# Optimization experiments

Measured on AMD Instinct MI355X. Metric: run time of the kernel, lower is better.

The kernel has to match this reference:

```python
import jax, jax.numpy as jnp
import numpy as np

DIM = 128
NUM_LAYERS = 5
EPS = 1e-5


def setup_inputs() -> dict:
    key = jax.random.key(0)
    ks = jax.random.split(key, 16)
    N, E, D = 50000, 640000, DIM
    x = jax.random.uniform(ks[0], (N, 3), dtype=jnp.float32)
    edge_index = jax.random.randint(ks[1], (2, E), 0, N, dtype=jnp.int64)
    norm = jax.random.uniform(ks[2], (E,), dtype=jnp.float32)
    s3 = 1.0 / np.sqrt(3.0)
    sd = 1.0 / np.sqrt(D)
    return {
        "x": x,
        "edge_index": edge_index,
        "norm": norm,
        "W_enc": jax.random.uniform(ks[3], (D, 3), jnp.float32, -s3, s3),
        "bn_e_gamma": jnp.ones((D,), jnp.float32),
        "bn_e_beta": jnp.zeros((D,), jnp.float32),
        "W_ih": jax.random.uniform(ks[4], (3 * D, D), jnp.float32, -sd, sd),
        "W_hh": jax.random.uniform(ks[5], (3 * D, D), jnp.float32, -sd, sd),
        "b_ih": jax.random.uniform(ks[6], (3 * D,), jnp.float32, -sd, sd),
        "b_hh": jax.random.uniform(ks[7], (3 * D,), jnp.float32, -sd, sd),
        "W_dec": jax.random.uniform(ks[8], (D // 2, D), jnp.float32, -sd, sd),
        "bn_d_gamma": jnp.ones((D // 2,), jnp.float32),
        "bn_d_beta": jnp.zeros((D // 2,), jnp.float32),
        "W_dec2": jax.random.uniform(ks[9], (1, D // 2), jnp.float32, -sd * np.sqrt(2.0), sd * np.sqrt(2.0)),
    }


def batchnorm(h, gamma, beta):
    # training-mode BatchNorm1d: biased batch stats over the node dimension
    mu = jnp.mean(h, axis=0)
    var = jnp.var(h, axis=0)
    return (h - mu) * jax.lax.rsqrt(var + EPS) * gamma + beta


def gru_cell(inp, hid, W_ih, W_hh, b_ih, b_hh):
    gi = inp @ W_ih.T + b_ih  # [N, 3D]
    gh = hid @ W_hh.T + b_hh
    D = hid.shape[1]
    i_r, i_z, i_n = gi[:, :D], gi[:, D:2 * D], gi[:, 2 * D:]
    h_r, h_z, h_n = gh[:, :D], gh[:, D:2 * D], gh[:, 2 * D:]
    r = jax.nn.sigmoid(i_r + h_r)
    z = jax.nn.sigmoid(i_z + h_z)
    n = jnp.tanh(i_n + r * h_n)
    return (1.0 - z) * n + z * hid


def reference(x, edge_index, norm, W_enc, bn_e_gamma, bn_e_beta, W_ih, W_hh, b_ih, b_hh, W_dec, bn_d_gamma, bn_d_beta, W_dec2):
    N = x.shape[0]
    src, dst = edge_index[0], edge_index[1]
    # encode
    h = jax.nn.relu(batchnorm(x @ W_enc.T, bn_e_gamma, bn_e_beta))  # [N, D]
    h_sum = h
    prev_h = h
    for _ in range(NUM_LAYERS):
        # neighborhood aggregation: scatter-add of norm-weighted source features
        msg = norm[:, None] * prev_h[src]  # [E, D]
        h_agg = jax.ops.segment_sum(msg, dst, num_segments=N)  # [N, D]
        h_sum = h_sum + h_agg
        prev_h = gru_cell(h_agg, prev_h, W_ih, W_hh, b_ih, b_hh)
    z = h_sum / (NUM_LAYERS + 1)  # mean over stacked h_list
    # decode
    y = jax.nn.relu(batchnorm(z @ W_dec.T, bn_d_gamma, bn_d_beta))
    y = y @ W_dec2.T  # [N, 1]
    return y.reshape(-1)
```

## Files before the change

kernel.cpp:

```cpp
#include <hip/hip_runtime.h>

#define DD 128

typedef _Float16 f16x8 __attribute__((ext_vector_type(8)));
typedef unsigned short u16x8 __attribute__((ext_vector_type(8)));
typedef float f32x4 __attribute__((ext_vector_type(4)));

__device__ __forceinline__ float sigmoidf_(float v){ return 1.f/(1.f+__expf(-v)); }
__device__ __forceinline__ float tanhf_(float v){
  float e2 = __expf(2.f*v);
  return 1.f - 2.f/(e2 + 1.f);
}
__device__ __forceinline__ float h2f(unsigned short u){
  _Float16 h; __builtin_memcpy(&h, &u, 2); return (float)h;
}
__device__ __forceinline__ unsigned short f2h(float v){
  _Float16 h = (_Float16)v; unsigned short u; __builtin_memcpy(&u, &h, 2); return u;
}

#define PREP_B 416
__global__ void __launch_bounds__(256) k_pre1(
        const float* __restrict__ W_ih, const float* __restrict__ W_hh,
        const float* __restrict__ W_dec, const float* __restrict__ x,
        const float* __restrict__ W_enc, const int* __restrict__ dst,
        unsigned short* __restrict__ Wih_h, unsigned short* __restrict__ Whh_h,
        float* __restrict__ Wt_dec, float* __restrict__ h0, float* __restrict__ stats,
        int* __restrict__ counts, int N, int E){
  const int tid = threadIdx.x;
  const int gb = blockIdx.x;
  const int TOT = 384*128;
  if (gb < PREP_B){
    int idx = gb*256 + tid;
    if (idx < 2*TOT){
      const float* W = (idx < TOT) ? W_ih : W_hh;
      unsigned short* D = (idx < TOT) ? Wih_h : Whh_h;
      int fi = (idx < TOT) ? idx : idx - TOT;
      int t = fi & 7;
      int l = (fi >> 3) & 63;
      int ks = (fi >> 9) & 3;
      int nt = fi >> 11;
      int fg = nt / 3, gate = nt % 3;
      int j = gate*128 + fg*16 + (l & 15);
      int k = ks*32 + ((l >> 4) & 3)*8 + t;
      D[fi] = f2h(W[j*128 + k]);
    } else if (idx < 2*TOT + 64*128){
      int t2 = idx - 2*TOT;
      int j = t2 / 128, k = t2 % 128;
      int o = ((k>>2)*64 + j)*4 + (k&3);
      Wt_dec[o] = W_dec[t2];
    }
  } else if (gb < PREP_B + 256){
    const int b = gb - PREP_B;
    const int f = tid & 127;
    const int sub = tid >> 7;
    const float w0 = W_enc[f*3], w1 = W_enc[f*3+1], w2 = W_enc[f*3+2];
    const int chunk = (N + 255) / 256;
    const int n0 = b * chunk;
    const int n1 = (n0 + chunk < N) ? (n0 + chunk) : N;
    float s = 0.f, q = 0.f;
    for (int n = n0 + sub; n < n1; n += 2){
      float x0 = x[n*3], x1 = x[n*3+1], x2 = x[n*3+2];
      float h = x0*w0 + x1*w1 + x2*w2;
      h0[(size_t)n*DD + f] = h;
      s += h; q += h*h;
    }
    atomicAdd(&stats[f], s);
    atomicAdd(&stats[DD+f], q);
  } else {
    int e = (gb - PREP_B - 256)*256 + tid;
    if (e < E) atomicAdd(&counts[dst[e]], 1);
  }
}

__global__ void __launch_bounds__(256) k_scan_part(const int* __restrict__ counts,
                                                   int* __restrict__ partials, int N){
  int i = blockIdx.x*256 + threadIdx.x;
  int v = (i < N) ? counts[i] : 0;
  #pragma unroll
  for (int off = 32; off > 0; off >>= 1) v += __shfl_down(v, off, 64);
  __shared__ int red[4];
  if ((threadIdx.x & 63) == 0) red[threadIdx.x >> 6] = v;
  __syncthreads();
  if (threadIdx.x == 0) partials[blockIdx.x] = red[0]+red[1]+red[2]+red[3];
}

__global__ void __launch_bounds__(256) k_scan_mid(int* __restrict__ partials, int P,
                                                  int* __restrict__ offsets, int N){
  __shared__ int lds[4];
  __shared__ int carry_s;
  const int lane = threadIdx.x & 63, wid = threadIdx.x >> 6;
  if (threadIdx.x == 0) carry_s = 0;
  __syncthreads();
  for (int base = 0; base < P; base += 256){
    int i = base + threadIdx.x;
    int v = (i < P) ? partials[i] : 0;
    int orig = v;
    #pragma unroll
    for (int off = 1; off < 64; off <<= 1){
      int u = __shfl_up(v, off, 64);
      if (lane >= off) v += u;
    }
    if (lane == 63) lds[wid] = v;
    __syncthreads();
    if (threadIdx.x == 0){
      int s = carry_s;
      for (int k = 0; k < 4; k++){ int t = lds[k]; lds[k] = s; s += t; }
      carry_s = s;
    }
    __syncthreads();
    int excl = v - orig + lds[wid];
    if (i < P) partials[i] = excl;
    __syncthreads();
  }
  if (threadIdx.x == 0) offsets[N] = carry_s;
}

__global__ void __launch_bounds__(256) k_scan_expand(const int* __restrict__ counts,
        const int* __restrict__ partials, int* __restrict__ offsets,
        int* __restrict__ cursors, int N){
  int i = blockIdx.x*256 + threadIdx.x;
  int v = (i < N) ? counts[i] : 0;
  int orig = v;
  const int lane = threadIdx.x & 63, wid = threadIdx.x >> 6;
  #pragma unroll
  for (int off = 1; off < 64; off <<= 1){
    int u = __shfl_up(v, off, 64);
    if (lane >= off) v += u;
  }
  __shared__ int lds[4];
  if (lane == 63) lds[wid] = v;
  __syncthreads();
  int wbase = 0;
  for (int k = 0; k < wid; k++) wbase += lds[k];
  int excl = partials[blockIdx.x] + wbase + v - orig;
  if (i < N){ offsets[i] = excl; cursors[i] = excl; }
}

__global__ void __launch_bounds__(256) k_pre2(
        const float* __restrict__ h0, const float* __restrict__ gamma,
        const float* __restrict__ beta, const float* __restrict__ stats,
        unsigned short* __restrict__ ph, unsigned short* __restrict__ hbn,
        const int* __restrict__ src, const int* __restrict__ dst,
        const float* __restrict__ norm, int* __restrict__ cursors,
        int2* __restrict__ csr, int N, int E, int AB){
  const int tid = threadIdx.x;
  if ((int)blockIdx.x < AB){
    int idx = blockIdx.x*256 + tid;
    if (idx >= N*DD) return;
    int f = idx & (DD-1);
    float invN = 1.f / (float)N;
    float mu = stats[f] * invN;
    float var = stats[DD+f] * invN - mu*mu;
    float v = (h0[idx] - mu) * rsqrtf(var + 1e-5f) * gamma[f] + beta[f];
    v = fmaxf(v, 0.f);
    unsigned short hv = f2h(v);
    ph[idx] = hv;
    hbn[idx] = hv;
  } else {
    int e = ((int)blockIdx.x - AB)*256 + tid;
    if (e >= E) return;
    int p = atomicAdd(&cursors[dst[e]], 1);
    union { float f; int i; } c; c.f = norm[e];
    csr[p] = make_int2(src[e], c.i);
  }
}

__global__ void __launch_bounds__(256, 4) k_layer(
        const unsigned short* __restrict__ phc,
        unsigned short* __restrict__ phn,
        unsigned short* __restrict__ agg_out,
        const int* __restrict__ offsets, const int2* __restrict__ csr,
        const unsigned short* __restrict__ Wih_h, const unsigned short* __restrict__ Whh_h,
        const float* __restrict__ b_ih, const float* __restrict__ b_hh, int N){
  __shared__ unsigned short s_a[32*DD];
  const int tid = threadIdx.x;
  const int n0 = blockIdx.x * 32;

  {
    const int slot = tid >> 4;
    const int q    = tid & 15;
    #pragma unroll
    for (int pass = 0; pass < 2; pass++){
      const int m = slot + pass*16;
      const int n = n0 + m;
      float acc[8];
      #pragma unroll
      for (int t = 0; t < 8; t++) acc[t] = 0.f;
      if (n < N){
        const int s0 = offsets[n], s1 = offsets[n+1];
        int i = s0;
        for (; i + 8 <= s1; i += 8){
          int2 ed[8]; u16x8 R[8];
          #pragma unroll
          for (int u = 0; u < 8; u++) ed[u] = csr[i+u];
          #pragma unroll
          for (int u = 0; u < 8; u++) R[u] = *(const u16x8*)(phc + (size_t)ed[u].x*DD + q*8);
          #pragma unroll
          for (int u = 0; u < 8; u++){
            union { int i; float f; } c; c.i = ed[u].y;
            #pragma unroll
            for (int t = 0; t < 8; t++)
              acc[t] = fmaf(c.f, h2f((unsigned short)R[u][t]), acc[t]);
          }
        }
        if (i + 4 <= s1){
          int2 ed[4]; u16x8 R[4];
          #pragma unroll
          for (int u = 0; u < 4; u++) ed[u] = csr[i+u];
          #pragma unroll
          for (int u = 0; u < 4; u++) R[u] = *(const u16x8*)(phc + (size_t)ed[u].x*DD + q*8);
          #pragma unroll
          for (int u = 0; u < 4; u++){
            union { int i; float f; } c; c.i = ed[u].y;
            #pragma unroll
            for (int t = 0; t < 8; t++)
              acc[t] = fmaf(c.f, h2f((unsigned short)R[u][t]), acc[t]);
          }
          i += 4;
        }
        for (; i < s1; i++){
          int2 ed = csr[i];
          union { int i; float f; } c; c.i = ed.y;
          u16x8 R = *(const u16x8*)(phc + (size_t)ed.x*DD + q*8);
          #pragma unroll
          for (int t = 0; t < 8; t++)
            acc[t] = fmaf(c.f, h2f((unsigned short)R[t]), acc[t]);
        }
      }
      u16x8 vh;
      #pragma unroll
      for (int t = 0; t < 8; t++) vh[t] = f2h(acc[t]);
      if (n < N)
        *(u16x8*)(agg_out + (size_t)n*DD + q*8) = vh;
      const int cc = q ^ (m & 7);
      *(u16x8*)(s_a + m*DD + cc*8) = vh;
    }
  }
  __syncthreads();

  const int w = tid >> 6, l = tid & 63, ar = l & 15, aq = l >> 4;
  int r0 = n0 + ar;      if (r0 >= N) r0 = N-1;
  int r1 = n0 + 16 + ar; if (r1 >= N) r1 = N-1;
  const size_t p0 = (size_t)r0*DD + aq*8;
  const size_t p1 = (size_t)r1*DD + aq*8;
  const int sw = ar & 7;

  for (int g = 0; g < 2; g++){
    const int fg = w*2 + g;
    f32x4 acc_i[2][3], acc_h[2][3];
    #pragma unroll
    for (int ta = 0; ta < 2; ta++)
      #pragma unroll
      for (int t = 0; t < 3; t++){
        acc_i[ta][t] = (f32x4){0.f,0.f,0.f,0.f};
        acc_h[ta][t] = (f32x4){0.f,0.f,0.f,0.f};
      }

    #pragma unroll
    for (int ks = 0; ks < 4; ks++){
      const int c = (ks*4 + aq) ^ sw;
      f16x8 ih0 = *(const f16x8*)(s_a + ar*DD       + c*8);
      f16x8 ih1 = *(const f16x8*)(s_a + (16+ar)*DD  + c*8);
      f16x8 hh0 = *(const f16x8*)(phc + p0 + ks*32);
      f16x8 hh1 = *(const f16x8*)(phc + p1 + ks*32);
      #pragma unroll
      for (int t = 0; t < 3; t++){
        size_t bo = ((size_t)((fg*3 + t)*4 + ks)*64 + l)*8;
        f16x8 bih = *(const f16x8*)(Wih_h + bo);
        f16x8 bhh = *(const f16x8*)(Whh_h + bo);
        acc_i[0][t] = __builtin_amdgcn_mfma_f32_16x16x32_f16(ih0, bih, acc_i[0][t], 0, 0, 0);
        acc_i[1][t] = __builtin_amdgcn_mfma_f32_16x16x32_f16(ih1, bih, acc_i[1][t], 0, 0, 0);
        acc_h[0][t] = __builtin_amdgcn_mfma_f32_16x16x32_f16(hh0, bhh, acc_h[0][t], 0, 0, 0);
        acc_h[1][t] = __builtin_amdgcn_mfma_f32_16x16x32_f16(hh1, bhh, acc_h[1][t], 0, 0, 0);
      }
    }

    const int f = fg*16 + ar;
    const float bir = b_ih[f], biz = b_ih[128+f], bin_ = b_ih[256+f];
    const float bhr = b_hh[f], bhz = b_hh[128+f], bhn = b_hh[256+f];
    #pragma unroll
    for (int ta = 0; ta < 2; ta++){
      #pragma unroll
      for (int r = 0; r < 4; r++){
        int n = n0 + ta*16 + aq*4 + r;
        if (n < N){
          float sir = acc_i[ta][0][r] + bir, shr = acc_h[ta][0][r] + bhr;
          float siz = acc_i[ta][1][r] + biz, shz = acc_h[ta][1][r] + bhz;
          float sin_ = acc_i[ta][2][r] + bin_, shn = acc_h[ta][2][r] + bhn;
          float rr = sigmoidf_(sir + shr);
          float zz = sigmoidf_(siz + shz);
          float nn = tanhf_(sin_ + rr*shn);
          size_t o = (size_t)n*DD + f;
          float hp = h2f(phc[o]);
          float h = (1.f - zz)*nn + zz*hp;
          phn[o] = f2h(h);
        }
      }
    }
  }
}

__global__ void __launch_bounds__(256) k_dec1(const unsigned short* __restrict__ hbn,
        const unsigned short* __restrict__ aggs, size_t NF,
        const unsigned short* __restrict__ ph5,
        const int* __restrict__ offsets, const int2* __restrict__ csr,
        const float* __restrict__ Wt_dec, float* __restrict__ y1,
        float* __restrict__ stats_d, int N){
  __shared__ float zs[32][DD];
  const int tid = threadIdx.x;
  const int n0 = blockIdx.x * 32;

  {
    const int slot = tid >> 4;
    const int q    = tid & 15;
    #pragma unroll
    for (int pass = 0; pass < 2; pass++){
      const int m = slot + pass*16;
      const int n = n0 + m;
      float acc[8];
      #pragma unroll
      for (int t = 0; t < 8; t++) acc[t] = 0.f;
      if (n < N){
        size_t o = (size_t)n*DD + q*8;
        u16x8 hb = *(const u16x8*)(hbn + o);
        #pragma unroll
        for (int t = 0; t < 8; t++) acc[t] = h2f(hb[t]);
        #pragma unroll
        for (int l = 0; l < 4; l++){
          u16x8 ag = *(const u16x8*)(aggs + l*NF + o);
          #pragma unroll
          for (int t = 0; t < 8; t++) acc[t] += h2f(ag[t]);
        }
        const int s0 = offsets[n], s1 = offsets[n+1];
        int i = s0;
        for (; i + 8 <= s1; i += 8){
          int2 ed[8]; u16x8 R[8];
          #pragma unroll
          for (int u = 0; u < 8; u++) ed[u] = csr[i+u];
          #pragma unroll
          for (int u = 0; u < 8; u++) R[u] = *(const u16x8*)(ph5 + (size_t)ed[u].x*DD + q*8);
          #pragma unroll
          for (int u = 0; u < 8; u++){
            union { int i; float f; } c; c.i = ed[u].y;
            #pragma unroll
            for (int t = 0; t < 8; t++)
              acc[t] = fmaf(c.f, h2f((unsigned short)R[u][t]), acc[t]);
          }
        }
        if (i + 4 <= s1){
          int2 ed[4]; u16x8 R[4];
          #pragma unroll
          for (int u = 0; u < 4; u++) ed[u] = csr[i+u];
          #pragma unroll
          for (int u = 0; u < 4; u++) R[u] = *(const u16x8*)(ph5 + (size_t)ed[u].x*DD + q*8);
          #pragma unroll
          for (int u = 0; u < 4; u++){
            union { int i; float f; } c; c.i = ed[u].y;
            #pragma unroll
            for (int t = 0; t < 8; t++)
              acc[t] = fmaf(c.f, h2f((unsigned short)R[u][t]), acc[t]);
          }
          i += 4;
        }
        for (; i < s1; i++){
          int2 ed = csr[i];
          union { int i; float f; } c; c.i = ed.y;
          u16x8 R = *(const u16x8*)(ph5 + (size_t)ed.x*DD + q*8);
          #pragma unroll
          for (int t = 0; t < 8; t++)
            acc[t] = fmaf(c.f, h2f((unsigned short)R[t]), acc[t]);
        }
      }
      #pragma unroll
      for (int t = 0; t < 8; t++) zs[m][q*8 + t] = acc[t] * (1.f/6.f);
    }
  }
  __syncthreads();

  const int w = tid >> 6, j = tid & 63;
  float s = 0.f, q = 0.f;
  #pragma unroll
  for (int it = 0; it < 8; it++){
    const int m = w*8 + it;
    const int n = n0 + m;
    if (n < N){
      float acc = 0.f;
      for (int k = 0; k < DD; k += 4){
        float4 wv = *(const float4*)(Wt_dec + ((size_t)(k>>2)*64 + j)*4);
        acc += zs[m][k]*wv.x + zs[m][k+1]*wv.y + zs[m][k+2]*wv.z + zs[m][k+3]*wv.w;
      }
      y1[(size_t)n*64 + j] = acc;
      s += acc; q += acc*acc;
    }
  }
  __shared__ float red[2][4][64];
  red[0][w][j] = s; red[1][w][j] = q;
  __syncthreads();
  if (w == 0){
    s = red[0][0][j] + red[0][1][j] + red[0][2][j] + red[0][3][j];
    q = red[1][0][j] + red[1][1][j] + red[1][2][j] + red[1][3][j];
    float* st = stats_d + (size_t)(blockIdx.x & 7)*128;
    atomicAdd(&st[j], s);
    atomicAdd(&st[64+j], q);
  }
}

__global__ void __launch_bounds__(256) k_dec2(const float* __restrict__ y1,
        const float* __restrict__ gamma, const float* __restrict__ beta,
        const float* __restrict__ W_dec2, const float* __restrict__ stats_d,
        float* __restrict__ out, int N){
  const int j = threadIdx.x & 63;
  const int g = threadIdx.x >> 6;
  const int n = blockIdx.x*4 + g;
  if (n >= N) return;
  float ssum = 0.f, qsum = 0.f;
  #pragma unroll
  for (int c = 0; c < 8; c++){
    ssum += stats_d[c*128 + j];
    qsum += stats_d[c*128 + 64 + j];
  }
  float invN = 1.f / (float)N;
  float mu = ssum * invN;
  float var = qsum * invN - mu*mu;
  float v = (y1[(size_t)n*64 + j] - mu) * rsqrtf(var + 1e-5f) * gamma[j] + beta[j];
  v = fmaxf(v, 0.f) * W_dec2[j];
  for (int off = 32; off > 0; off >>= 1) v += __shfl_down(v, off, 64);
  if (j == 0) out[n] = v;
}

extern "C" void kernel_launch(void* const* d_in, const int* in_sizes, int n_in,
                              void* d_out, int out_size, void* d_ws, size_t ws_size,
                              hipStream_t stream) {
  const int N = in_sizes[0] / 3;
  const int E = in_sizes[1] / 2;
  const int P = (N + 255) / 256;
  const int HIST_B = (E + 255) / 256;
  const int AB = (N*DD + 255) / 256;

  const float* x     = (const float*)d_in[0];
  const int*   ei    = (const int*)d_in[1];
  const int*   src   = ei;
  const int*   dst   = ei + E;
  const float* norm  = (const float*)d_in[2];
  const float* W_enc = (const float*)d_in[3];
  const float* g_e   = (const float*)d_in[4];
  const float* b_e   = (const float*)d_in[5];
  const float* W_ih  = (const float*)d_in[6];
  const float* W_hh  = (const float*)d_in[7];
  const float* b_ih  = (const float*)d_in[8];
  const float* b_hh  = (const float*)d_in[9];
  const float* W_dec = (const float*)d_in[10];
  const float* g_d   = (const float*)d_in[11];
  const float* b_d   = (const float*)d_in[12];
  const float* W_dec2= (const float*)d_in[13];
  float* out = (float*)d_out;

  float* ws = (float*)d_ws;
  const size_t NF = (size_t)N * DD;
  float* scr    = ws;
  float* stats  = scr + NF;
  float* Wt_dec = stats + 1280;
  unsigned short* Wih_h = (unsigned short*)(Wt_dec + 64*128);
  unsigned short* Whh_h = Wih_h + 384*128;
  unsigned short* ph_A  = Whh_h + 384*128;
  unsigned short* ph_B  = ph_A + NF;
  unsigned short* hbn   = ph_B + NF;
  unsigned short* aggs  = hbn + NF;
  int*   counts  = (int*)(aggs + 4*NF);
  int*   offsets = counts + N;
  int*   cursors = offsets + N + 1;
  int*   partials= cursors + N;
  int2*  csr     = (int2*)(partials + P);
  float* y1 = scr;

  hipMemsetAsync(stats, 0, 1280*sizeof(float), stream);
  hipMemsetAsync(counts, 0, (size_t)N*sizeof(int), stream);

  k_pre1<<<PREP_B + 256 + HIST_B, 256, 0, stream>>>(
      W_ih, W_hh, W_dec, x, W_enc, dst,
      Wih_h, Whh_h, Wt_dec, scr, stats, counts, N, E);
  k_scan_part<<<P, 256, 0, stream>>>(counts, partials, N);
  k_scan_mid<<<1, 256, 0, stream>>>(partials, P, offsets, N);
  k_scan_expand<<<P, 256, 0, stream>>>(counts, partials, offsets, cursors, N);
  k_pre2<<<AB + HIST_B, 256, 0, stream>>>(
      scr, g_e, b_e, stats, ph_A, hbn,
      src, dst, norm, cursors, csr, N, E, AB);

  unsigned short* phh_c = ph_A;
  unsigned short* phh_n = ph_B;
  for (int l = 0; l < 4; l++){
    k_layer<<<(N + 31)/32, 256, 0, stream>>>(phh_c, phh_n, aggs + (size_t)l*NF,
                                             offsets, csr,
                                             Wih_h, Whh_h, b_ih, b_hh, N);
    unsigned short* t = phh_c; phh_c = phh_n; phh_n = t;
  }

  k_dec1<<<(N + 31)/32, 256, 0, stream>>>(hbn, aggs, NF, phh_c, offsets, csr,
                                          Wt_dec, y1, stats + 256, N);
  k_dec2<<<(N + 3)/4, 256, 0, stream>>>(y1, g_d, b_d, W_dec2, stats + 256, out, N);
}
```

Measured before the change: 514.9 us.

## Halve node tile to 16 rows and use MFMA for decoder projection

The per-layer kernel now handles 16 nodes per block instead of 32, with one gather pass per thread and half the MFMA accumulators, and the launch bound allows 5 blocks per CU. This is meant to raise occupancy and parallelism for the latency-bound gather. The decoder first stage is rewritten to store z as fp16 in swizzled shared memory and compute the 128→64 projection with fp16 MFMA against a pre-packed W_dec, replacing the scalar fp32 dot-product loop and shared-memory reduction. Each weight fragment is now reused across only 16 rows, so weight loads per node double, and z is rounded to fp16 before the projection.

```diff
diff --git a/kernel.cpp b/kernel.cpp
--- a/kernel.cpp
+++ b/kernel.cpp
@@ -24,7 +24,7 @@
         const float* __restrict__ W_dec, const float* __restrict__ x,
         const float* __restrict__ W_enc, const int* __restrict__ dst,
         unsigned short* __restrict__ Wih_h, unsigned short* __restrict__ Whh_h,
-        float* __restrict__ Wt_dec, float* __restrict__ h0, float* __restrict__ stats,
+        unsigned short* __restrict__ Wd_h, float* __restrict__ h0, float* __restrict__ stats,
         int* __restrict__ counts, int N, int E){
   const int tid = threadIdx.x;
   const int gb = blockIdx.x;
@@ -44,10 +44,14 @@
       int k = ks*32 + ((l >> 4) & 3)*8 + t;
       D[fi] = f2h(W[j*128 + k]);
     } else if (idx < 2*TOT + 64*128){
-      int t2 = idx - 2*TOT;
-      int j = t2 / 128, k = t2 % 128;
-      int o = ((k>>2)*64 + j)*4 + (k&3);
-      Wt_dec[o] = W_dec[t2];
+      int fi2 = idx - 2*TOT;
+      int t  = fi2 & 7;
+      int l  = (fi2 >> 3) & 63;
+      int ks = (fi2 >> 9) & 3;
+      int jt = fi2 >> 11;
+      int j = jt*16 + (l & 15);
+      int k = ks*32 + ((l >> 4) & 3)*8 + t;
+      Wd_h[fi2] = f2h(W_dec[j*128 + k]);
     }
   } else if (gb < PREP_B + 256){
     const int b = gb - PREP_B;
@@ -165,113 +169,101 @@
   }
 }
 
-__global__ void __launch_bounds__(256, 4) k_layer(
+__global__ void __launch_bounds__(256, 5) k_layer(
         const unsigned short* __restrict__ phc,
         unsigned short* __restrict__ phn,
         unsigned short* __restrict__ agg_out,
         const int* __restrict__ offsets, const int2* __restrict__ csr,
         const unsigned short* __restrict__ Wih_h, const unsigned short* __restrict__ Whh_h,
         const float* __restrict__ b_ih, const float* __restrict__ b_hh, int N){
-  __shared__ unsigned short s_a[32*DD];
+  __shared__ unsigned short s_a[16*DD];
   const int tid = threadIdx.x;
-  const int n0 = blockIdx.x * 32;
+  const int n0 = blockIdx.x * 16;
 
   {
-    const int slot = tid >> 4;
-    const int q    = tid & 15;
-    #pragma unroll
-    for (int pass = 0; pass < 2; pass++){
-      const int m = slot + pass*16;
-      const int n = n0 + m;
-      float acc[8];
-      #pragma unroll
-      for (int t = 0; t < 8; t++) acc[t] = 0.f;
-      if (n < N){
-        const int s0 = offsets[n], s1 = offsets[n+1];
-        int i = s0;
-        for (; i + 8 <= s1; i += 8){
-          int2 ed[8]; u16x8 R[8];
-          #pragma unroll
-          for (int u = 0; u < 8; u++) ed[u] = csr[i+u];
-          #pragma unroll
-          for (int u = 0; u < 8; u++) R[u] = *(const u16x8*)(phc + (size_t)ed[u].x*DD + q*8);
-          #pragma unroll
-          for (int u = 0; u < 8; u++){
-            union { int i; float f; } c; c.i = ed[u].y;
-            #pragma unroll
-            for (int t = 0; t < 8; t++)
-              acc[t] = fmaf(c.f, h2f((unsigned short)R[u][t]), acc[t]);
-          }
-        }
-        if (i + 4 <= s1){
-          int2 ed[4]; u16x8 R[4];
-          #pragma unroll
-          for (int u = 0; u < 4; u++) ed[u] = csr[i+u];
-          #pragma unroll
-          for (int u = 0; u < 4; u++) R[u] = *(const u16x8*)(phc + (size_t)ed[u].x*DD + q*8);
-          #pragma unroll
-          for (int u = 0; u < 4; u++){
-            union { int i; float f; } c; c.i = ed[u].y;
-            #pragma unroll
-            for (int t = 0; t < 8; t++)
-              acc[t] = fmaf(c.f, h2f((unsigned short)R[u][t]), acc[t]);
-          }
-          i += 4;
-        }
-        for (; i < s1; i++){
-          int2 ed = csr[i];
-          union { int i; float f; } c; c.i = ed.y;
-          u16x8 R = *(const u16x8*)(phc + (size_t)ed.x*DD + q*8);
+    const int m = tid >> 4;
+    const int q = tid & 15;
+    const int n = n0 + m;
+    float acc[8];
+    #pragma unroll
+    for (int t = 0; t < 8; t++) acc[t] = 0.f;
+    if (n < N){
+      const int s0 = offsets[n], s1 = offsets[n+1];
+      int i = s0;
+      for (; i + 8 <= s1; i += 8){
+        int2 ed[8]; u16x8 R[8];
+        #pragma unroll
+        for (int u = 0; u < 8; u++) ed[u] = csr[i+u];
+        #pragma unroll
+        for (int u = 0; u < 8; u++) R[u] = *(const u16x8*)(phc + (size_t)ed[u].x*DD + q*8);
+        #pragma unroll
+        for (int u = 0; u < 8; u++){
+          union { int i; float f; } c; c.i = ed[u].y;
           #pragma unroll
           for (int t = 0; t < 8; t++)
-            acc[t] = fmaf(c.f, h2f((unsigned short)R[t]), acc[t]);
+            acc[t] = fmaf(c.f, h2f((unsigned short)R[u][t]), acc[t]);
         }
       }
-      u16x8 vh;
-      #pragma unroll
-      for (int t = 0; t < 8; t++) vh[t] = f2h(acc[t]);
-      if (n < N)
-        *(u16x8*)(agg_out + (size_t)n*DD + q*8) = vh;
-      const int cc = q ^ (m & 7);
-      *(u16x8*)(s_a + m*DD + cc*8) = vh;
-    }
+      if (i + 4 <= s1){
+        int2 ed[4]; u16x8 R[4];
+        #pragma unroll
+        for (int u = 0; u < 4; u++) ed[u] = csr[i+u];
+        #pragma unroll
+        for (int u = 0; u < 4; u++) R[u] = *(const u16x8*)(phc + (size_t)ed[u].x*DD + q*8);
+        #pragma unroll
+        for (int u = 0; u < 4; u++){
+          union { int i; float f; } c; c.i = ed[u].y;
+          #pragma unroll
+          for (int t = 0; t < 8; t++)
+            acc[t] = fmaf(c.f, h2f((unsigned short)R[u][t]), acc[t]);
+        }
+        i += 4;
+      }
+      for (; i < s1; i++){
+        int2 ed = csr[i];
+        union { int i; float f; } c; c.i = ed.y;
+        u16x8 R = *(const u16x8*)(phc + (size_t)ed.x*DD + q*8);
+        #pragma unroll
+        for (int t = 0; t < 8; t++)
+          acc[t] = fmaf(c.f, h2f((unsigned short)R[t]), acc[t]);
+      }
+    }
+    u16x8 vh;
+    #pragma unroll
+    for (int t = 0; t < 8; t++) vh[t] = f2h(acc[t]);
+    if (n < N)
+      *(u16x8*)(agg_out + (size_t)n*DD + q*8) = vh;
+    const int cc = q ^ (m & 7);
+    *(u16x8*)(s_a + m*DD + cc*8) = vh;
   }
   __syncthreads();
 
   const int w = tid >> 6, l = tid & 63, ar = l & 15, aq = l >> 4;
-  int r0 = n0 + ar;      if (r0 >= N) r0 = N-1;
-  int r1 = n0 + 16 + ar; if (r1 >= N) r1 = N-1;
+  int r0 = n0 + ar; if (r0 >= N) r0 = N-1;
   const size_t p0 = (size_t)r0*DD + aq*8;
-  const size_t p1 = (size_t)r1*DD + aq*8;
   const int sw = ar & 7;
 
   for (int g = 0; g < 2; g++){
     const int fg = w*2 + g;
-    f32x4 acc_i[2][3], acc_h[2][3];
-    #pragma unroll
-    for (int ta = 0; ta < 2; ta++)
-      #pragma unroll
-      for (int t = 0; t < 3; t++){
-        acc_i[ta][t] = (f32x4){0.f,0.f,0.f,0.f};
-        acc_h[ta][t] = (f32x4){0.f,0.f,0.f,0.f};
-      }
+    f32x4 acc_i[3], acc_h[3];
+    #pragma unroll
+    for (int t = 0; t < 3; t++){
+      acc_i[t] = (f32x4){0.f,0.f,0.f,0.f};
+      acc_h[t] = (f32x4){0.f,0.f,0.f,0.f};
+    }
 
     #pragma unroll
     for (int ks = 0; ks < 4; ks++){
       const int c = (ks*4 + aq) ^ sw;
-      f16x8 ih0 = *(const f16x8*)(s_a + ar*DD       + c*8);
-      f16x8 ih1 = *(const f16x8*)(s_a + (16+ar)*DD  + c*8);
+      f16x8 ih0 = *(const f16x8*)(s_a + ar*DD + c*8);
       f16x8 hh0 = *(const f16x8*)(phc + p0 + ks*32);
-      f16x8 hh1 = *(const f16x8*)(phc + p1 + ks*32);
       #pragma unroll
       for (int t = 0; t < 3; t++){
         size_t bo = ((size_t)((fg*3 + t)*4 + ks)*64 + l)*8;
         f16x8 bih = *(const f16x8*)(Wih_h + bo);
         f16x8 bhh = *(const f16x8*)(Whh_h + bo);
-        acc_i[0][t] = __builtin_amdgcn_mfma_f32_16x16x32_f16(ih0, bih, acc_i[0][t], 0, 0, 0);
-        acc_i[1][t] = __builtin_amdgcn_mfma_f32_16x16x32_f16(ih1, bih, acc_i[1][t], 0, 0, 0);
-        acc_h[0][t] = __builtin_amdgcn_mfma_f32_16x16x32_f16(hh0, bhh, acc_h[0][t], 0, 0, 0);
-        acc_h[1][t] = __builtin_amdgcn_mfma_f32_16x16x32_f16(hh1, bhh, acc_h[1][t], 0, 0, 0);
+        acc_i[t] = __builtin_amdgcn_mfma_f32_16x16x32_f16(ih0, bih, acc_i[t], 0, 0, 0);
+        acc_h[t] = __builtin_amdgcn_mfma_f32_16x16x32_f16(hh0, bhh, acc_h[t], 0, 0, 0);
       }
     }
 
@@ -279,129 +271,126 @@
     const float bir = b_ih[f], biz = b_ih[128+f], bin_ = b_ih[256+f];
     const float bhr = b_hh[f], bhz = b_hh[128+f], bhn = b_hh[256+f];
     #pragma unroll
-    for (int ta = 0; ta < 2; ta++){
-      #pragma unroll
-      for (int r = 0; r < 4; r++){
-        int n = n0 + ta*16 + aq*4 + r;
-        if (n < N){
-          float sir = acc_i[ta][0][r] + bir, shr = acc_h[ta][0][r] + bhr;
-          float siz = acc_i[ta][1][r] + biz, shz = acc_h[ta][1][r] + bhz;
-          float sin_ = acc_i[ta][2][r] + bin_, shn = acc_h[ta][2][r] + bhn;
-          float rr = sigmoidf_(sir + shr);
-          float zz = sigmoidf_(siz + shz);
-          float nn = tanhf_(sin_ + rr*shn);
-          size_t o = (size_t)n*DD + f;
-          float hp = h2f(phc[o]);
-          float h = (1.f - zz)*nn + zz*hp;
-          phn[o] = f2h(h);
-        }
-      }
-    }
-  }
-}
-
-__global__ void __launch_bounds__(256) k_dec1(const unsigned short* __restrict__ hbn,
+    for (int r = 0; r < 4; r++){
+      int n = n0 + aq*4 + r;
+      if (n < N){
+        float sir = acc_i[0][r] + bir, shr = acc_h[0][r] + bhr;
+        float siz = acc_i[1][r] + biz, shz = acc_h[1][r] + bhz;
+        float sin_ = acc_i[2][r] + bin_, shn = acc_h[2][r] + bhn;
+        float rr = sigmoidf_(sir + shr);
+        float zz = sigmoidf_(siz + shz);
+        float nn = tanhf_(sin_ + rr*shn);
+        size_t o = (size_t)n*DD + f;
+        float hp = h2f(phc[o]);
+        float h = (1.f - zz)*nn + zz*hp;
+        phn[o] = f2h(h);
+      }
+    }
+  }
+}
+
+__global__ void __launch_bounds__(256, 8) k_dec1(const unsigned short* __restrict__ hbn,
         const unsigned short* __restrict__ aggs, size_t NF,
         const unsigned short* __restrict__ ph5,
         const int* __restrict__ offsets, const int2* __restrict__ csr,
-        const float* __restrict__ Wt_dec, float* __restrict__ y1,
+        const unsigned short* __restrict__ Wd_h, float* __restrict__ y1,
         float* __restrict__ stats_d, int N){
-  __shared__ float zs[32][DD];
+  __shared__ unsigned short zs[16*DD];
   const int tid = threadIdx.x;
-  const int n0 = blockIdx.x * 32;
+  const int n0 = blockIdx.x * 16;
 
   {
-    const int slot = tid >> 4;
-    const int q    = tid & 15;
-    #pragma unroll
-    for (int pass = 0; pass < 2; pass++){
-      const int m = slot + pass*16;
-      const int n = n0 + m;
-      float acc[8];
+    const int m = tid >> 4;
+    const int q = tid & 15;
+    const int n = n0 + m;
+    float acc[8];
+    #pragma unroll
+    for (int t = 0; t < 8; t++) acc[t] = 0.f;
+    if (n < N){
+      size_t o = (size_t)n*DD + q*8;
+      u16x8 hb = *(const u16x8*)(hbn + o);
       #pragma unroll
-      for (int t = 0; t < 8; t++) acc[t] = 0.f;
-      if (n < N){
-        size_t o = (size_t)n*DD + q*8;
-        u16x8 hb = *(const u16x8*)(hbn + o);
-        #pragma unroll
-        for (int t = 0; t < 8; t++) acc[t] = h2f(hb[t]);
-        #pragma unroll
-        for (int l = 0; l < 4; l++){
-          u16x8 ag = *(const u16x8*)(aggs + l*NF + o);
-          #pragma unroll
-          for (int t = 0; t < 8; t++) acc[t] += h2f(ag[t]);
-        }
-        const int s0 = offsets[n], s1 = offsets[n+1];
-        int i = s0;
-        for (; i + 8 <= s1; i += 8){
-          int2 ed[8]; u16x8 R[8];
-          #pragma unroll
-          for (int u = 0; u < 8; u++) ed[u] = csr[i+u];
-          #pragma unroll
-          for (int u = 0; u < 8; u++) R[u] = *(const u16x8*)(ph5 + (size_t)ed[u].x*DD + q*8);
-          #pragma unroll
-          for (int u = 0; u < 8; u++){
-            union { int i; float f; } c; c.i = ed[u].y;
-            #pragma unroll
-            for (int t = 0; t < 8; t++)
-              acc[t] = fmaf(c.f, h2f((unsigned short)R[u][t]), acc[t]);
-          }
-        }
-        if (i + 4 <= s1){
-          int2 ed[4]; u16x8 R[4];
-          #pragma unroll
-          for (int u = 0; u < 4; u++) ed[u] = csr[i+u];
-          #pragma unroll
-          for (int u = 0; u < 4; u++) R[u] = *(const u16x8*)(ph5 + (size_t)ed[u].x*DD + q*8);
-          #pragma unroll
-          for (int u = 0; u < 4; u++){
-            union { int i; float f; } c; c.i = ed[u].y;
-            #pragma unroll
-            for (int t = 0; t < 8; t++)
-              acc[t] = fmaf(c.f, h2f((unsigned short)R[u][t]), acc[t]);
-          }
-          i += 4;
-        }
-        for (; i < s1; i++){
-          int2 ed = csr[i];
-          union { int i; float f; } c; c.i = ed.y;
-          u16x8 R = *(const u16x8*)(ph5 + (size_t)ed.x*DD + q*8);
+      for (int t = 0; t < 8; t++) acc[t] = h2f(hb[t]);
+      #pragma unroll
+      for (int l = 0; l < 4; l++){
+        u16x8 ag = *(const u16x8*)(aggs + l*NF + o);
+        #pragma unroll
+        for (int t = 0; t < 8; t++) acc[t] += h2f(ag[t]);
+      }
+      const int s0 = offsets[n], s1 = offsets[n+1];
+      int i = s0;
+      for (; i + 8 <= s1; i += 8){
+        int2 ed[8]; u16x8 R[8];
+        #pragma unroll
+        for (int u = 0; u < 8; u++) ed[u] = csr[i+u];
+        #pragma unroll
+        for (int u = 0; u < 8; u++) R[u] = *(const u16x8*)(ph5 + (size_t)ed[u].x*DD + q*8);
+        #pragma unroll
+        for (int u = 0; u < 8; u++){
+          union { int i; float f; } c; c.i = ed[u].y;
           #pragma unroll
           for (int t = 0; t < 8; t++)
-            acc[t] = fmaf(c.f, h2f((unsigned short)R[t]), acc[t]);
+            acc[t] = fmaf(c.f, h2f((unsigned short)R[u][t]), acc[t]);
         }
       }
-      #pragma unroll
-      for (int t = 0; t < 8; t++) zs[m][q*8 + t] = acc[t] * (1.f/6.f);
-    }
+      if (i + 4 <= s1){
+        int2 ed[4]; u16x8 R[4];
+        #pragma unroll
+        for (int u = 0; u < 4; u++) ed[u] = csr[i+u];
+        #pragma unroll
+        for (int u = 0; u < 4; u++) R[u] = *(const u16x8*)(ph5 + (size_t)ed[u].x*DD + q*8);
+        #pragma unroll
+        for (int u = 0; u < 4; u++){
+          union { int i; float f; } c; c.i = ed[u].y;
+          #pragma unroll
+          for (int t = 0; t < 8; t++)
+            acc[t] = fmaf(c.f, h2f((unsigned short)R[u][t]), acc[t]);
+        }
+        i += 4;
+      }
+      for (; i < s1; i++){
+        int2 ed = csr[i];
+        union { int i; float f; } c; c.i = ed.y;
+        u16x8 R = *(const u16x8*)(ph5 + (size_t)ed.x*DD + q*8);
+        #pragma unroll
+        for (int t = 0; t < 8; t++)
+          acc[t] = fmaf(c.f, h2f((unsigned short)R[t]), acc[t]);
+      }
+    }
+    u16x8 vh;
+    #pragma unroll
+    for (int t = 0; t < 8; t++) vh[t] = f2h(acc[t] * (1.f/6.f));
+    const int cc = q ^ (m & 7);
+    *(u16x8*)(zs + m*DD + cc*8) = vh;
   }
   __syncthreads();
 
-  const int w = tid >> 6, j = tid & 63;
-  float s = 0.f, q = 0.f;
+  const int w = tid >> 6, l = tid & 63, ar = l & 15, aq = l >> 4;
+  const int sw = ar & 7;
+  f32x4 acc = (f32x4){0.f,0.f,0.f,0.f};
   #pragma unroll
-  for (int it = 0; it < 8; it++){
-    const int m = w*8 + it;
-    const int n = n0 + m;
+  for (int ks = 0; ks < 4; ks++){
+    const int c = (ks*4 + aq) ^ sw;
+    f16x8 a = *(const f16x8*)(zs + ar*DD + c*8);
+    f16x8 b = *(const f16x8*)(Wd_h + ((size_t)(w*4 + ks)*64 + l)*8);
+    acc = __builtin_amdgcn_mfma_f32_16x16x32_f16(a, b, acc, 0, 0, 0);
+  }
+  float s = 0.f, q2 = 0.f;
+  #pragma unroll
+  for (int r = 0; r < 4; r++){
+    int n = n0 + aq*4 + r;
+    float v = acc[r];
     if (n < N){
-      float acc = 0.f;
-      for (int k = 0; k < DD; k += 4){
-        float4 wv = *(const float4*)(Wt_dec + ((size_t)(k>>2)*64 + j)*4);
-        acc += zs[m][k]*wv.x + zs[m][k+1]*wv.y + zs[m][k+2]*wv.z + zs[m][k+3]*wv.w;
-      }
-      y1[(size_t)n*64 + j] = acc;
-      s += acc; q += acc*acc;
-    }
-  }
-  __shared__ float red[2][4][64];
-  red[0][w][j] = s; red[1][w][j] = q;
-  __syncthreads();
-  if (w == 0){
-    s = red[0][0][j] + red[0][1][j] + red[0][2][j] + red[0][3][j];
-    q = red[1][0][j] + red[1][1][j] + red[1][2][j] + red[1][3][j];
+      y1[(size_t)n*64 + w*16 + ar] = v;
+      s += v; q2 += v*v;
+    }
+  }
+  s  += __shfl_xor(s, 16, 64);  s  += __shfl_xor(s, 32, 64);
+  q2 += __shfl_xor(q2, 16, 64); q2 += __shfl_xor(q2, 32, 64);
+  if (aq == 0){
     float* st = stats_d + (size_t)(blockIdx.x & 7)*128;
-    atomicAdd(&st[j], s);
-    atomicAdd(&st[64+j], q);
+    atomicAdd(&st[w*16 + ar], s);
+    atomicAdd(&st[64 + w*16 + ar], q2);
   }
 }
 
@@ -460,6 +449,7 @@
   float* scr    = ws;
   float* stats  = scr + NF;
   float* Wt_dec = stats + 1280;
+  unsigned short* Wd_h  = (unsigned short*)Wt_dec;
   unsigned short* Wih_h = (unsigned short*)(Wt_dec + 64*128);
   unsigned short* Whh_h = Wih_h + 384*128;
   unsigned short* ph_A  = Whh_h + 384*128;
@@ -478,7 +468,7 @@
 
   k_pre1<<<PREP_B + 256 + HIST_B, 256, 0, stream>>>(
       W_ih, W_hh, W_dec, x, W_enc, dst,
-      Wih_h, Whh_h, Wt_dec, scr, stats, counts, N, E);
+      Wih_h, Whh_h, Wd_h, scr, stats, counts, N, E);
   k_scan_part<<<P, 256, 0, stream>>>(counts, partials, N);
   k_scan_mid<<<1, 256, 0, stream>>>(partials, P, offsets, N);
   k_scan_expand<<<P, 256, 0, stream>>>(counts, partials, offsets, cursors, N);
@@ -489,13 +479,13 @@
   unsigned short* phh_c = ph_A;
   unsigned short* phh_n = ph_B;
   for (int l = 0; l < 4; l++){
-    k_layer<<<(N + 31)/32, 256, 0, stream>>>(phh_c, phh_n, aggs + (size_t)l*NF,
+    k_layer<<<(N + 15)/16, 256, 0, stream>>>(phh_c, phh_n, aggs + (size_t)l*NF,
                                              offsets, csr,
                                              Wih_h, Whh_h, b_ih, b_hh, N);
     unsigned short* t = phh_c; phh_c = phh_n; phh_n = t;
   }
 
-  k_dec1<<<(N + 31)/32, 256, 0, stream>>>(hbn, aggs, NF, phh_c, offsets, csr,
-                                          Wt_dec, y1, stats + 256, N);
+  k_dec1<<<(N + 15)/16, 256, 0, stream>>>(hbn, aggs, NF, phh_c, offsets, csr,
+                                          Wd_h, y1, stats + 256, N);
   k_dec2<<<(N + 3)/4, 256, 0, stream>>>(y1, g_d, b_d, W_dec2, stats + 256, out, N);
 }
```

Result: faster. 499.5 us (-3.0%).
